# Performance work log

Measured on AMD Instinct MI355X. Metric: run time of the kernel, lower is better.

## Reference

```python
import jax, jax.numpy as jnp
import numpy as np

N = 20000          # nodes
E = 320000         # edges (avg degree 16)
FS = 1000          # feature_size (resnet feature width)
IN = 250 + FS + 250 + 85 * 3  # 1755, actual concat width


def setup_inputs() -> dict:
    key = jax.random.key(0)
    ks = jax.random.split(key, 16)
    # structured node feature matrix x: [layer_id | resnet(1000) | rel_size | rgb(3)]
    layer = jax.random.randint(ks[0], (N, 1), 1, 4).astype(jnp.float32)      # {1,2,3}
    resnet = jax.random.normal(ks[1], (N, FS), jnp.float32)
    rel = jax.random.uniform(ks[2], (N, 1), jnp.float32)                      # [0,1] -> idx 0..10
    colors = jax.random.randint(ks[3], (N, 3), 0, 256).astype(jnp.float32)
    x = jnp.concatenate([layer, resnet, rel, colors], axis=1)  # [N,1005]
    edge_index = jax.random.randint(ks[4], (2, E), 0, N)
    edge_attr = jax.random.uniform(ks[5], (E,), jnp.float32)

    def lin(k, fi, fo):
        return jax.random.normal(k, (fi, fo), jnp.float32) / np.sqrt(fi).astype(np.float32)

    return {
        "x": x,
        "edge_index": edge_index,
        "edge_attr": edge_attr,
        "layer_table": jax.random.normal(ks[6], (3, 250), jnp.float32),
        "rel_table": jax.random.normal(ks[7], (11, 250), jnp.float32),
        "color_table": jax.random.normal(ks[8], (256, 85), jnp.float32),
        "W1": lin(ks[9], IN, 512), "b1": jnp.zeros((512,), jnp.float32),
        "W2": lin(ks[10], 512, 256), "b2": jnp.zeros((256,), jnp.float32),
        "W3": lin(ks[11], 256, 64), "b3": jnp.zeros((64,), jnp.float32),
        "Wp": lin(ks[12], 64, 3), "bp": jnp.zeros((3,), jnp.float32),
    }


def _gcn_conv(h, src, dst, ew, W, b):
    # PyG GCNConv: h' = D^{-1/2} (A + I) D^{-1/2} (h W) + b, with edge weights ew
    h = h @ W
    deg = jax.ops.segment_sum(ew, dst, num_segments=N) + 1.0  # +1 for self-loop weight
    dinv = jnp.where(deg > 0.0, jax.lax.rsqrt(deg), 0.0)
    norm = dinv[src] * ew * dinv[dst]                          # [E]
    agg = jax.ops.segment_sum(h[src] * norm[:, None], dst, num_segments=N)
    agg = agg + h * (dinv * dinv)[:, None]                     # self-loop term
    return agg + b


def reference(x, edge_index, edge_attr, layer_table, rel_table, color_table,
              W1, b1, W2, b2, W3, b3, Wp, bp):
    src, dst = edge_index[0], edge_index[1]
    li = (x[:, 0] - 1.0).astype(jnp.int32)                      # layer id 0..2
    le = layer_table[li]                                        # [N,250]
    resnet = x[:, 1:FS + 1]                                     # [N,1000]
    ri = jnp.round(jnp.abs(x[:, FS + 1]) * 10.0).astype(jnp.int32)
    re = rel_table[ri]                                          # [N,250]
    ci = x[:, -3:].astype(jnp.int32)
    ce = color_table[ci].reshape(x.shape[0], -1)                # [N,255]
    h = jnp.concatenate([le, resnet, re, ce], axis=1)           # [N,1755]

    lrelu = lambda v: jax.nn.leaky_relu(v, 0.01)
    h = lrelu(_gcn_conv(h, src, dst, edge_attr, W1, b1))
    h = lrelu(_gcn_conv(h, src, dst, edge_attr, W2, b2))
    h = lrelu(_gcn_conv(h, src, dst, edge_attr, W3, b3))
    return h @ Wp + bp                                          # [N,3]
```

## Files before the change

### kernel.cpp

```cpp
#include <hip/hip_runtime.h>
#include <hip/hip_bf16.h>

#define NNODES 20000
#define NEDGES 320000
#define XW 1005
#define MP 20096

typedef __attribute__((ext_vector_type(8))) short short8;
typedef __attribute__((ext_vector_type(4))) float f32x4;
typedef __attribute__((ext_vector_type(4))) unsigned short u16x4;

typedef const __attribute__((address_space(1))) short8* g8cp;

__device__ inline void split1(float v, unsigned short& h, unsigned short& l) {
    unsigned u = __float_as_uint(v);
    h = (unsigned short)(u >> 16);
    float hf = __uint_as_float(u & 0xffff0000u);
    l = (unsigned short)(__float_as_uint(v - hf) >> 16);
}

#define PB_EDGE  1250
#define PB_IDX   1329
#define PB_A1    21329
#define PB_BT1   21841
#define PB_BT2   21969
#define PB_BT3   21985
#define PB_TAB   23549

__device__ inline void bt_split_body(int g, const float* __restrict__ W, int ldw,
                                     int koff, int K, int Kp, int Ncols,
                                     unsigned short* __restrict__ Bh,
                                     unsigned short* __restrict__ Bl) {
    int kp4 = Kp >> 2;
    if (g >= Ncols * kp4) return;
    int n = g / kp4, c4 = (g % kp4) << 2;
    u16x4 h, l;
#pragma unroll
    for (int i = 0; i < 4; ++i) {
        int k = c4 + i;
        float v = (k < K) ? W[(size_t)(koff + k) * ldw + n] : 0.0f;
        unsigned short hh, ll;
        split1(v, hh, ll);
        h[i] = (short)hh; l[i] = (short)ll;
    }
    *(u16x4*)&Bh[(size_t)n * Kp + c4] = h;
    *(u16x4*)&Bl[(size_t)n * Kp + c4] = l;
}

__global__ __launch_bounds__(256) void prep_kernel(
    const float* __restrict__ x, const int* __restrict__ ei, const float* __restrict__ ea,
    const float* __restrict__ layer_table, const float* __restrict__ rel_table,
    const float* __restrict__ color_table,
    const float* __restrict__ W1, const float* __restrict__ W2, const float* __restrict__ W3,
    float* __restrict__ deg, int* __restrict__ counts, int* __restrict__ idx8,
    unsigned short* __restrict__ A1h, unsigned short* __restrict__ A1l,
    unsigned short* __restrict__ Bt1h, unsigned short* __restrict__ Bt1l,
    unsigned short* __restrict__ Bt2h, unsigned short* __restrict__ Bt2l,
    unsigned short* __restrict__ Bt3h, unsigned short* __restrict__ Bt3l,
    float* __restrict__ T) {
    const int b = blockIdx.x;
    const int t = threadIdx.x;
    if (b < PB_EDGE) {
        int e = b * 256 + t;
        if (e >= NEDGES) return;
        int dst = ei[NEDGES + e];
        atomicAdd(&deg[dst], ea[e]);
        atomicAdd(&counts[dst], 1);
    } else if (b < PB_IDX) {
        int i = (b - PB_EDGE) * 256 + t;
        if (i >= NNODES) return;
        const float* r = x + (size_t)i * XW;
        idx8[i * 8 + 0] = (int)(r[0] - 1.0f);
        idx8[i * 8 + 1] = (int)rintf(fabsf(r[1001]) * 10.0f);
        idx8[i * 8 + 2] = (int)r[1002];
        idx8[i * 8 + 3] = (int)r[1003];
        idx8[i * 8 + 4] = (int)r[1004];
    } else if (b < PB_A1) {
        int row = b - PB_IDX;
        int c4 = t << 2;
        const float* xp = x + (size_t)row * XW + 1 + c4;
        u16x4 h, l;
#pragma unroll
        for (int i = 0; i < 4; ++i) {
            float v = (c4 + i < 1000) ? xp[i] : 0.0f;
            unsigned short hh, ll;
            split1(v, hh, ll);
            h[i] = (short)hh; l[i] = (short)ll;
        }
        *(u16x4*)&A1h[(size_t)row * 1024 + c4] = h;
        *(u16x4*)&A1l[(size_t)row * 1024 + c4] = l;
    } else if (b < PB_BT1) {
        bt_split_body((b - PB_A1) * 256 + t, W1, 512, 250, 1000, 1024, 512, Bt1h, Bt1l);
    } else if (b < PB_BT2) {
        bt_split_body((b - PB_BT1) * 256 + t, W2, 256, 0, 512, 512, 256, Bt2h, Bt2l);
    } else if (b < PB_BT3) {
        bt_split_body((b - PB_BT2) * 256 + t, W3, 64, 0, 256, 256, 64, Bt3h, Bt3l);
    } else {
        int g = (b - PB_BT3) * 256 + t;
        if (g >= 782 * 512) return;
        int row = g >> 9, col = g & 511;
        float acc = 0.0f;
        if (row < 3) {
            for (int k = 0; k < 250; ++k)
                acc += layer_table[row * 250 + k] * W1[(size_t)k * 512 + col];
        } else if (row < 14) {
            int r = row - 3;
            for (int k = 0; k < 250; ++k)
                acc += rel_table[r * 250 + k] * W1[(size_t)(1250 + k) * 512 + col];
        } else {
            int r = row - 14;
            int j = r >> 8, v = r & 255;
            int base = 1500 + 85 * j;
            for (int k = 0; k < 85; ++k)
                acc += color_table[v * 85 + k] * W1[(size_t)(base + k) * 512 + col];
        }
        T[(size_t)row * 512 + col] = acc;
    }
}


__global__ __launch_bounds__(1024) void scan_p1_kernel(const int* __restrict__ counts,
                                                       int* __restrict__ bsum,
                                                       const float* __restrict__ deg,
                                                       float* __restrict__ dinv, int n) {
    int b = blockIdx.x;
    if (b < 20) {
        __shared__ int ws[16];
        int t = threadIdx.x, lane = t & 63, wid = t >> 6;
        int i = b * 1024 + t;
        int v = (i < n) ? counts[i] : 0;
#pragma unroll
        for (int d = 32; d; d >>= 1) v += __shfl_down(v, d, 64);
        if (lane == 0) ws[wid] = v;
        __syncthreads();
        if (wid == 0) {
            int s = (lane < 16) ? ws[lane] : 0;
#pragma unroll
            for (int d = 8; d; d >>= 1) s += __shfl_down(s, d, 64);
            if (lane == 0) bsum[b] = s;
        }
    } else {
        int i = (b - 20) * 1024 + threadIdx.x;
        if (i < n) { float d = deg[i] + 1.0f; dinv[i] = 1.0f / sqrtf(d); }
    }
}

__global__ void scan_p2_kernel(const int* __restrict__ bsum, int* __restrict__ boffs,
                               int* __restrict__ offs, int n, int nb) {
    int lane = threadIdx.x;
    int v = (lane < nb) ? bsum[lane] : 0;
    int xv = v;
#pragma unroll
    for (int d = 1; d < 64; d <<= 1) {
        int u = __shfl_up(xv, d, 64);
        if (lane >= d) xv += u;
    }
    if (lane < nb) boffs[lane] = xv - v;
    if (lane == nb - 1) offs[n] = xv;
}

__global__ __launch_bounds__(1024) void scan_p3_kernel(const int* __restrict__ counts,
                                                       const int* __restrict__ boffs,
                                                       int* __restrict__ offs, int n) {
    __shared__ int wsum[16], wpre[16];
    int t = threadIdx.x, lane = t & 63, wid = t >> 6;
    int i = blockIdx.x * 1024 + t;
    int v = (i < n) ? counts[i] : 0;
    int xv = v;
#pragma unroll
    for (int d = 1; d < 64; d <<= 1) {
        int u = __shfl_up(xv, d, 64);
        if (lane >= d) xv += u;
    }
    if (lane == 63) wsum[wid] = xv;
    __syncthreads();
    if (wid == 0) {
        int s = (lane < 16) ? wsum[lane] : 0;
#pragma unroll
        for (int d = 1; d < 16; d <<= 1) {
            int u = __shfl_up(s, d, 64);
            if (lane >= d) s += u;
        }
        if (lane < 16) wpre[lane] = s;
    }
    __syncthreads();
    int prefix = boffs[blockIdx.x] + (wid > 0 ? wpre[wid - 1] : 0);
    if (i < n) offs[i] = prefix + xv - v;
}

__global__ void scatter_kernel(const int* __restrict__ ei, const float* __restrict__ ea,
                               const float* __restrict__ dinv, const int* __restrict__ offs,
                               int* __restrict__ cursor, int* __restrict__ csr_src,
                               float* __restrict__ csr_norm, int E) {
    int e = blockIdx.x * 256 + threadIdx.x;
    if (e >= E) return;
    int src = ei[e];
    int dst = ei[E + e];
    int slot = offs[dst] + atomicAdd(&cursor[dst], 1);
    csr_src[slot] = src;
    csr_norm[slot] = dinv[src] * ea[e] * dinv[dst];
}


template <int BN, int NCB, bool EMB>
__global__ __launch_bounds__(256, 3) void gemm_split_kernel(
    const unsigned short* __restrict__ Ah, const unsigned short* __restrict__ Al, int Kp,
    const unsigned short* __restrict__ Bh, const unsigned short* __restrict__ Bl,
    float* __restrict__ C, int ldc, int M,
    const float* __restrict__ T, const int* __restrict__ idx8) {
    constexpr int NT = BN / 32;
    constexpr int BJ = BN / 64;
    __shared__ __align__(16) unsigned short sAh[128 * 32];
    __shared__ __align__(16) unsigned short sAl[128 * 32];
    __shared__ __align__(16) unsigned short sBh[BN * 32];
    __shared__ __align__(16) unsigned short sBl[BN * 32];

    const int t = threadIdx.x;
    const int lane = t & 63;
    const int w = t >> 6;
    const int wr = w >> 1, wc = w & 1;
    const int l15 = lane & 15, quad = lane >> 4;

    const int total = gridDim.x;
    const int per = total >> 3;
    const int bid = blockIdx.x;
    const int tile = (bid < (per << 3)) ? ((bid & 7) * per + (bid >> 3)) : bid;
    const int row0 = (tile / NCB) * 128;
    const int col0 = (tile % NCB) * BN;

    const int si_r = lane >> 2;
    const int si_s = lane & 3;
    const int schunk = si_s ^ ((si_r >> 1) & 3);
    const int sw = (quad ^ ((l15 >> 1) & 3)) * 8;

    const unsigned short* gA[2][2];
    int aoff[2];
#pragma unroll
    for (int j = 0; j < 2; ++j) {
        int ra = w * 32 + j * 16 + si_r;
        size_t e = (size_t)(row0 + ra) * Kp + schunk * 8;
        gA[j][0] = Ah + e; gA[j][1] = Al + e;
        aoff[j] = (w * 32 + j * 16 + si_r) * 32 + si_s * 8;
    }
    const unsigned short* gB[BJ][2];
    int boff[BJ];
#pragma unroll
    for (int j = 0; j < BJ; ++j) {
        int rb = w * (BN / 4) + j * 16 + si_r;
        size_t e = (size_t)(col0 + rb) * Kp + schunk * 8;
        gB[j][0] = Bh + e; gB[j][1] = Bl + e;
        boff[j] = (w * (BN / 4) + j * 16 + si_r) * 32 + si_s * 8;
    }

    f32x4 acc[4][NT];
#pragma unroll
    for (int i = 0; i < 4; ++i)
#pragma unroll
        for (int j = 0; j < NT; ++j)
            acc[i][j] = (f32x4){0.f, 0.f, 0.f, 0.f};

    const int nit = Kp / 32;

    short8 pA[2][2], pB[BJ][2];
#pragma unroll
    for (int j = 0; j < 2; ++j) {
        pA[j][0] = *(g8cp)(const void*)(gA[j][0]);
        pA[j][1] = *(g8cp)(const void*)(gA[j][1]);
    }
#pragma unroll
    for (int j = 0; j < BJ; ++j) {
        pB[j][0] = *(g8cp)(const void*)(gB[j][0]);
        pB[j][1] = *(g8cp)(const void*)(gB[j][1]);
    }

    for (int kt = 0; kt < nit; ++kt) {
#pragma unroll
        for (int j = 0; j < 2; ++j) {
            *(short8*)&sAh[aoff[j]] = pA[j][0];
            *(short8*)&sAl[aoff[j]] = pA[j][1];
        }
#pragma unroll
        for (int j = 0; j < BJ; ++j) {
            *(short8*)&sBh[boff[j]] = pB[j][0];
            *(short8*)&sBl[boff[j]] = pB[j][1];
        }
        if (kt + 1 < nit) {
            const int kb = (kt + 1) * 32;
#pragma unroll
            for (int j = 0; j < 2; ++j) {
                pA[j][0] = *(g8cp)(const void*)(gA[j][0] + kb);
                pA[j][1] = *(g8cp)(const void*)(gA[j][1] + kb);
            }
#pragma unroll
            for (int j = 0; j < BJ; ++j) {
                pB[j][0] = *(g8cp)(const void*)(gB[j][0] + kb);
                pB[j][1] = *(g8cp)(const void*)(gB[j][1] + kb);
            }
        }
        __builtin_amdgcn_s_waitcnt(0xC07F);
        __builtin_amdgcn_s_barrier();
        __builtin_amdgcn_sched_barrier(0);

        short8 fah[4], fal[4], fbh[NT], fbl[NT];
#pragma unroll
        for (int mt = 0; mt < 4; ++mt) {
            int off = (wr * 64 + mt * 16 + l15) * 32 + sw;
            fah[mt] = *(const short8*)&sAh[off];
            fal[mt] = *(const short8*)&sAl[off];
        }
#pragma unroll
        for (int nt = 0; nt < NT; ++nt) {
            int off = (wc * (BN / 2) + nt * 16 + l15) * 32 + sw;
            fbh[nt] = *(const short8*)&sBh[off];
            fbl[nt] = *(const short8*)&sBl[off];
        }
#pragma unroll
        for (int mt = 0; mt < 4; ++mt)
#pragma unroll
            for (int nt = 0; nt < NT; ++nt)
                acc[mt][nt] = __builtin_amdgcn_mfma_f32_16x16x32_bf16(fah[mt], fbh[nt], acc[mt][nt], 0, 0, 0);
#pragma unroll
        for (int mt = 0; mt < 4; ++mt)
#pragma unroll
            for (int nt = 0; nt < NT; ++nt)
                acc[mt][nt] = __builtin_amdgcn_mfma_f32_16x16x32_bf16(fah[mt], fbl[nt], acc[mt][nt], 0, 0, 0);
#pragma unroll
        for (int mt = 0; mt < 4; ++mt)
#pragma unroll
            for (int nt = 0; nt < NT; ++nt)
                acc[mt][nt] = __builtin_amdgcn_mfma_f32_16x16x32_bf16(fal[mt], fbh[nt], acc[mt][nt], 0, 0, 0);
        if (kt + 1 < nit) __builtin_amdgcn_s_barrier();
    }

#pragma unroll
    for (int mt = 0; mt < 4; ++mt)
#pragma unroll
        for (int r = 0; r < 4; ++r) {
            int row = row0 + wr * 64 + mt * 16 + quad * 4 + r;
            if (row >= M) continue;
            if (EMB) {
                const int* ix = idx8 + row * 8;
                const float* t0 = T + (size_t)ix[0] * 512;
                const float* t1 = T + (size_t)(3 + ix[1]) * 512;
                const float* t2 = T + (size_t)(14 + ix[2]) * 512;
                const float* t3 = T + (size_t)(270 + ix[3]) * 512;
                const float* t4 = T + (size_t)(526 + ix[4]) * 512;
#pragma unroll
                for (int nt = 0; nt < NT; ++nt) {
                    int col = col0 + wc * (BN / 2) + nt * 16 + l15;
                    float e = t0[col] + t1[col] + t2[col] + t3[col] + t4[col];
                    C[(size_t)row * ldc + col] = acc[mt][nt][r] + e;
                }
            } else {
#pragma unroll
                for (int nt = 0; nt < NT; ++nt) {
                    int col = col0 + wc * (BN / 2) + nt * 16 + l15;
                    C[(size_t)row * ldc + col] = acc[mt][nt][r];
                }
            }
        }
}


template <int F, int CW, bool SPLIT>
__global__ __launch_bounds__(256) void agg_cols_kernel(
    const float* __restrict__ H, const float* __restrict__ dinv,
    const int* __restrict__ offs, const int* __restrict__ csr_src,
    const float* __restrict__ csr_norm, const float* __restrict__ bias,
    float* __restrict__ outf, unsigned short* __restrict__ Hh,
    unsigned short* __restrict__ Hl, int n_nodes) {
    constexpr int LPN = CW / 4;
    constexpr int NPB = 256 / LPN;
    constexpr int NCH = F / CW;
    constexpr int ECAP = 2048;
    __shared__ int   se[ECAP];
    __shared__ float sn[ECAP];

    const int chunk = blockIdx.x & (NCH - 1);
    const int nb    = blockIdx.x / NCH;
    const int n0 = nb * NPB;
    const int n1 = min(n0 + NPB, n_nodes);
    if (n0 >= n_nodes) return;

    const int estart = offs[n0];
    const int eend   = offs[n1];
    const int ecnt   = eend - estart;
    const bool inlds = (ecnt <= ECAP);
    if (inlds) {
        for (int i = threadIdx.x; i < ecnt; i += 256) {
            se[i] = csr_src[estart + i];
            sn[i] = csr_norm[estart + i];
        }
    }
    __syncthreads();

    const int n = n0 + threadIdx.x / LPN;
    if (n >= n_nodes) return;
    const int lane = threadIdx.x % LPN;
    const int c = chunk * CW + lane * 4;

    float di = dinv[n];
    float s = di * di;
    float4 h = *(const float4*)(H + (size_t)n * F + c);
    float4 acc = make_float4(h.x * s, h.y * s, h.z * s, h.w * s);
    int e0 = offs[n], e1 = offs[n + 1];
    if (inlds) {
        for (int e = e0 - estart; e < e1 - estart; ++e) {
            int src = se[e];
            float w = sn[e];
            float4 v = *(const float4*)(H + (size_t)src * F + c);
            acc.x += v.x * w; acc.y += v.y * w; acc.z += v.z * w; acc.w += v.w * w;
        }
    } else {
        for (int e = e0; e < e1; ++e) {
            int src = csr_src[e];
            float w = csr_norm[e];
            float4 v = *(const float4*)(H + (size_t)src * F + c);
            acc.x += v.x * w; acc.y += v.y * w; acc.z += v.z * w; acc.w += v.w * w;
        }
    }
    float4 b = *(const float4*)(bias + c);
    acc.x += b.x; acc.y += b.y; acc.z += b.z; acc.w += b.w;
    acc.x = acc.x > 0.f ? acc.x : 0.01f * acc.x;
    acc.y = acc.y > 0.f ? acc.y : 0.01f * acc.y;
    acc.z = acc.z > 0.f ? acc.z : 0.01f * acc.z;
    acc.w = acc.w > 0.f ? acc.w : 0.01f * acc.w;
    if (SPLIT) {
        u16x4 hh, ll;
        unsigned short a, bb;
        split1(acc.x, a, bb); hh[0] = (short)a; ll[0] = (short)bb;
        split1(acc.y, a, bb); hh[1] = (short)a; ll[1] = (short)bb;
        split1(acc.z, a, bb); hh[2] = (short)a; ll[2] = (short)bb;
        split1(acc.w, a, bb); hh[3] = (short)a; ll[3] = (short)bb;
        *(u16x4*)(Hh + (size_t)n * F + c) = hh;
        *(u16x4*)(Hl + (size_t)n * F + c) = ll;
    } else {
        *(float4*)(outf + (size_t)n * F + c) = acc;
    }
}


__global__ void proj_kernel(const float* __restrict__ H, const float* __restrict__ Wp,
                            const float* __restrict__ bp, float* __restrict__ out, int n_nodes) {
    int t = blockIdx.x * 192 + threadIdx.x;
    int n = t / 3, j = t % 3;
    if (n >= n_nodes) return;
    float acc = bp[j];
    const float* h = H + (size_t)n * 64;
    for (int c = 0; c < 64; ++c) acc += h[c] * Wp[c * 3 + j];
    out[n * 3 + j] = acc;
}


static inline size_t aln(size_t v) { return (v + 255) & ~(size_t)255; }

extern "C" void kernel_launch(void* const* d_in, const int* in_sizes, int n_in,
                              void* d_out, int out_size, void* d_ws, size_t ws_size,
                              hipStream_t stream) {
    const float* x           = (const float*)d_in[0];
    const int*   edge_index  = (const int*)d_in[1];
    const float* edge_attr   = (const float*)d_in[2];
    const float* layer_table = (const float*)d_in[3];
    const float* rel_table   = (const float*)d_in[4];
    const float* color_table = (const float*)d_in[5];
    const float* W1 = (const float*)d_in[6];
    const float* b1 = (const float*)d_in[7];
    const float* W2 = (const float*)d_in[8];
    const float* b2 = (const float*)d_in[9];
    const float* W3 = (const float*)d_in[10];
    const float* b3 = (const float*)d_in[11];
    const float* Wp = (const float*)d_in[12];
    const float* bp = (const float*)d_in[13];
    float* out = (float*)d_out;

    const int N = NNODES, E = NEDGES;

    char* p = (char*)d_ws;
    float* deg      = (float*)p;
    int*   counts   = (int*)(p + (size_t)N * 4);
    int*   cursor   = (int*)(p + (size_t)N * 8);     p += aln((size_t)N * 12);
    float* dinv     = (float*)p; p += aln((size_t)N * 4);
    float* T        = (float*)p; p += aln((size_t)782 * 512 * 4);
    float* csr_norm = (float*)p; p += aln((size_t)E * 4);
    float* C        = (float*)p; p += aln((size_t)MP * 512 * 4);
    unsigned short* BIG = (unsigned short*)p; p += aln((size_t)MP * 2048 * 2);
    unsigned short* Bt1h = (unsigned short*)p; p += aln((size_t)512 * 1024 * 2);
    unsigned short* Bt1l = (unsigned short*)p; p += aln((size_t)512 * 1024 * 2);
    unsigned short* Bt2h = (unsigned short*)p; p += aln((size_t)256 * 512 * 2);
    unsigned short* Bt2l = (unsigned short*)p; p += aln((size_t)256 * 512 * 2);
    unsigned short* Bt3h = (unsigned short*)p; p += aln((size_t)64 * 256 * 2);
    unsigned short* Bt3l = (unsigned short*)p; p += aln((size_t)64 * 256 * 2);
    int*   csr_src  = (int*)p;   p += aln((size_t)E * 4);
    int*   idx8     = (int*)p;   p += aln((size_t)N * 8 * 4);
    int*   offs     = (int*)p;   p += aln((size_t)(N + 1) * 4);
    int*   bsum     = (int*)p;   p += aln((size_t)32 * 4);
    int*   boffs    = (int*)p;   p += aln((size_t)32 * 4);

    unsigned short* A1h = BIG;
    unsigned short* A1l = BIG + (size_t)MP * 1024;
    unsigned short* H2h = BIG;
    unsigned short* H2l = BIG + (size_t)MP * 512;
    unsigned short* H3h = BIG + (size_t)MP * 1024;
    unsigned short* H3l = BIG + (size_t)MP * 1024 + (size_t)MP * 256;
    float*          H4  = (float*)(BIG + (size_t)MP * 1536);

    hipMemsetAsync(deg, 0, (size_t)N * 12, stream);

    prep_kernel<<<PB_TAB, 256, 0, stream>>>(
        x, edge_index, edge_attr, layer_table, rel_table, color_table,
        W1, W2, W3, deg, counts, idx8,
        A1h, A1l, Bt1h, Bt1l, Bt2h, Bt2l, Bt3h, Bt3l, T);

    scan_p1_kernel<<<40, 1024, 0, stream>>>(counts, bsum, deg, dinv, N);
    scan_p2_kernel<<<1, 64, 0, stream>>>(bsum, boffs, offs, N, 20);
    scan_p3_kernel<<<20, 1024, 0, stream>>>(counts, boffs, offs, N);
    scatter_kernel<<<(E + 255) / 256, 256, 0, stream>>>(edge_index, edge_attr, dinv, offs,
                                                        cursor, csr_src, csr_norm, E);

    const int nrb = MP / 128;

    {
        gemm_split_kernel<128, 4, true><<<nrb * 4, 256, 0, stream>>>(
            A1h, A1l, 1024, Bt1h, Bt1l, C, 512, N, T, idx8);
        int nblocks = (N + 15) / 16;
        agg_cols_kernel<512, 64, true><<<8 * nblocks, 256, 0, stream>>>(
            C, dinv, offs, csr_src, csr_norm, b1, nullptr, H2h, H2l, N);
    }
    {
        gemm_split_kernel<128, 2, false><<<nrb * 2, 256, 0, stream>>>(
            H2h, H2l, 512, Bt2h, Bt2l, C, 256, N, nullptr, nullptr);
        int nblocks = (N + 31) / 32;
        agg_cols_kernel<256, 32, true><<<8 * nblocks, 256, 0, stream>>>(
            C, dinv, offs, csr_src, csr_norm, b2, nullptr, H3h, H3l, N);
    }
    {
        gemm_split_kernel<64, 1, false><<<nrb, 256, 0, stream>>>(
            H3h, H3l, 256, Bt3h, Bt3l, C, 64, N, nullptr, nullptr);
        int nblocks = (N + 63) / 64;
        agg_cols_kernel<64, 16, false><<<4 * nblocks, 256, 0, stream>>>(
            C, dinv, offs, csr_src, csr_norm, b3, H4, nullptr, nullptr, N);
    }
    proj_kernel<<<(N * 3 + 191) / 192, 192, 0, stream>>>(H4, Wp, bp, out, N);
}
```

Baseline: 447.7 us.

## Load GEMM A fragments directly from global, double-buffer B, fuse projection into aggregation

The split-bf16 GEMM stops staging the A tile through shared memory. Each wave now loads its MFMA A fragments straight from global memory, interleaved with the MFMA groups, while B is double-buffered in LDS with a two-step-ahead register prefetch and one barrier per iteration. Separately, the final 64->3 projection is fused into the last aggregation kernel through a lane shuffle reduction, which removes the H4 intermediate and the proj_kernel launch. The direct A loads are uncoalesced per-lane 16-byte reads that rely on cache hits, and the wave is exposed to their global latency inside the MFMA loop.

```diff
diff --git a/kernel.cpp b/kernel.cpp
--- a/kernel.cpp
+++ b/kernel.cpp
@@ -203,17 +203,15 @@
 
 
 template <int BN, int NCB, bool EMB>
-__global__ __launch_bounds__(256, 3) void gemm_split_kernel(
+__global__ __launch_bounds__(256, 3) void gemm_direct_kernel(
     const unsigned short* __restrict__ Ah, const unsigned short* __restrict__ Al, int Kp,
     const unsigned short* __restrict__ Bh, const unsigned short* __restrict__ Bl,
     float* __restrict__ C, int ldc, int M,
     const float* __restrict__ T, const int* __restrict__ idx8) {
     constexpr int NT = BN / 32;
     constexpr int BJ = BN / 64;
-    __shared__ __align__(16) unsigned short sAh[128 * 32];
-    __shared__ __align__(16) unsigned short sAl[128 * 32];
-    __shared__ __align__(16) unsigned short sBh[BN * 32];
-    __shared__ __align__(16) unsigned short sBl[BN * 32];
+    __shared__ __align__(16) unsigned short sBh[2][BN * 32];
+    __shared__ __align__(16) unsigned short sBl[2][BN * 32];
 
     const int t = threadIdx.x;
     const int lane = t & 63;
@@ -233,15 +231,14 @@
     const int schunk = si_s ^ ((si_r >> 1) & 3);
     const int sw = (quad ^ ((l15 >> 1) & 3)) * 8;
 
-    const unsigned short* gA[2][2];
-    int aoff[2];
-#pragma unroll
-    for (int j = 0; j < 2; ++j) {
-        int ra = w * 32 + j * 16 + si_r;
-        size_t e = (size_t)(row0 + ra) * Kp + schunk * 8;
-        gA[j][0] = Ah + e; gA[j][1] = Al + e;
-        aoff[j] = (w * 32 + j * 16 + si_r) * 32 + si_s * 8;
-    }
+    const unsigned short* pAh[4]; const unsigned short* pAl[4];
+#pragma unroll
+    for (int mt = 0; mt < 4; ++mt) {
+        int r = row0 + wr * 64 + mt * 16 + l15;
+        size_t o = (size_t)r * Kp + quad * 8;
+        pAh[mt] = Ah + o; pAl[mt] = Al + o;
+    }
+
     const unsigned short* gB[BJ][2];
     int boff[BJ];
 #pragma unroll
@@ -261,75 +258,99 @@
 
     const int nit = Kp / 32;
 
-    short8 pA[2][2], pB[BJ][2];
-#pragma unroll
-    for (int j = 0; j < 2; ++j) {
-        pA[j][0] = *(g8cp)(const void*)(gA[j][0]);
-        pA[j][1] = *(g8cp)(const void*)(gA[j][1]);
-    }
+    short8 pB[BJ][2];
 #pragma unroll
     for (int j = 0; j < BJ; ++j) {
         pB[j][0] = *(g8cp)(const void*)(gB[j][0]);
         pB[j][1] = *(g8cp)(const void*)(gB[j][1]);
     }
+#pragma unroll
+    for (int j = 0; j < BJ; ++j) {
+        *(short8*)&sBh[0][boff[j]] = pB[j][0];
+        *(short8*)&sBl[0][boff[j]] = pB[j][1];
+    }
+#pragma unroll
+    for (int j = 0; j < BJ; ++j) {
+        pB[j][0] = *(g8cp)(const void*)(gB[j][0] + 32);
+        pB[j][1] = *(g8cp)(const void*)(gB[j][1] + 32);
+    }
+    __builtin_amdgcn_s_waitcnt(0xC07F);
+    __builtin_amdgcn_s_barrier();
+    __builtin_amdgcn_sched_barrier(0);
 
     for (int kt = 0; kt < nit; ++kt) {
-#pragma unroll
-        for (int j = 0; j < 2; ++j) {
-            *(short8*)&sAh[aoff[j]] = pA[j][0];
-            *(short8*)&sAl[aoff[j]] = pA[j][1];
-        }
+        const int cur = kt & 1, nxt = cur ^ 1;
+        const int kbA = kt * 32;
 #pragma unroll
         for (int j = 0; j < BJ; ++j) {
-            *(short8*)&sBh[boff[j]] = pB[j][0];
-            *(short8*)&sBl[boff[j]] = pB[j][1];
-        }
-        if (kt + 1 < nit) {
-            const int kb = (kt + 1) * 32;
-#pragma unroll
-            for (int j = 0; j < 2; ++j) {
-                pA[j][0] = *(g8cp)(const void*)(gA[j][0] + kb);
-                pA[j][1] = *(g8cp)(const void*)(gA[j][1] + kb);
+            *(short8*)&sBh[nxt][boff[j]] = pB[j][0];
+            *(short8*)&sBl[nxt][boff[j]] = pB[j][1];
+        }
+        short8 fa0h = *(g8cp)(const void*)(pAh[0] + kbA);
+        short8 fa0l = *(g8cp)(const void*)(pAl[0] + kbA);
+        short8 fa1h = *(g8cp)(const void*)(pAh[1] + kbA);
+        short8 fa1l = *(g8cp)(const void*)(pAl[1] + kbA);
+        {
+            const int kb2 = (kt + 2 < nit) ? (kt + 2) * 32 : 0;
+#pragma unroll
+            for (int j = 0; j < BJ; ++j) {
+                pB[j][0] = *(g8cp)(const void*)(gB[j][0] + kb2);
+                pB[j][1] = *(g8cp)(const void*)(gB[j][1] + kb2);
             }
-#pragma unroll
-            for (int j = 0; j < BJ; ++j) {
-                pB[j][0] = *(g8cp)(const void*)(gB[j][0] + kb);
-                pB[j][1] = *(g8cp)(const void*)(gB[j][1] + kb);
-            }
-        }
-        __builtin_amdgcn_s_waitcnt(0xC07F);
-        __builtin_amdgcn_s_barrier();
-        __builtin_amdgcn_sched_barrier(0);
-
-        short8 fah[4], fal[4], fbh[NT], fbl[NT];
-#pragma unroll
-        for (int mt = 0; mt < 4; ++mt) {
-            int off = (wr * 64 + mt * 16 + l15) * 32 + sw;
-            fah[mt] = *(const short8*)&sAh[off];
-            fal[mt] = *(const short8*)&sAl[off];
-        }
+        }
+        short8 fbh[NT], fbl[NT];
 #pragma unroll
         for (int nt = 0; nt < NT; ++nt) {
             int off = (wc * (BN / 2) + nt * 16 + l15) * 32 + sw;
-            fbh[nt] = *(const short8*)&sBh[off];
-            fbl[nt] = *(const short8*)&sBl[off];
-        }
-#pragma unroll
-        for (int mt = 0; mt < 4; ++mt)
-#pragma unroll
-            for (int nt = 0; nt < NT; ++nt)
-                acc[mt][nt] = __builtin_amdgcn_mfma_f32_16x16x32_bf16(fah[mt], fbh[nt], acc[mt][nt], 0, 0, 0);
-#pragma unroll
-        for (int mt = 0; mt < 4; ++mt)
-#pragma unroll
-            for (int nt = 0; nt < NT; ++nt)
-                acc[mt][nt] = __builtin_amdgcn_mfma_f32_16x16x32_bf16(fah[mt], fbl[nt], acc[mt][nt], 0, 0, 0);
-#pragma unroll
-        for (int mt = 0; mt < 4; ++mt)
-#pragma unroll
-            for (int nt = 0; nt < NT; ++nt)
-                acc[mt][nt] = __builtin_amdgcn_mfma_f32_16x16x32_bf16(fal[mt], fbh[nt], acc[mt][nt], 0, 0, 0);
-        if (kt + 1 < nit) __builtin_amdgcn_s_barrier();
+            fbh[nt] = *(const short8*)&sBh[cur][off];
+            fbl[nt] = *(const short8*)&sBl[cur][off];
+        }
+#pragma unroll
+        for (int nt = 0; nt < NT; ++nt)
+            acc[0][nt] = __builtin_amdgcn_mfma_f32_16x16x32_bf16(fa0h, fbh[nt], acc[0][nt], 0, 0, 0);
+#pragma unroll
+        for (int nt = 0; nt < NT; ++nt)
+            acc[0][nt] = __builtin_amdgcn_mfma_f32_16x16x32_bf16(fa0h, fbl[nt], acc[0][nt], 0, 0, 0);
+#pragma unroll
+        for (int nt = 0; nt < NT; ++nt)
+            acc[0][nt] = __builtin_amdgcn_mfma_f32_16x16x32_bf16(fa0l, fbh[nt], acc[0][nt], 0, 0, 0);
+        fa0h = *(g8cp)(const void*)(pAh[2] + kbA);
+        fa0l = *(g8cp)(const void*)(pAl[2] + kbA);
+#pragma unroll
+        for (int nt = 0; nt < NT; ++nt)
+            acc[1][nt] = __builtin_amdgcn_mfma_f32_16x16x32_bf16(fa1h, fbh[nt], acc[1][nt], 0, 0, 0);
+#pragma unroll
+        for (int nt = 0; nt < NT; ++nt)
+            acc[1][nt] = __builtin_amdgcn_mfma_f32_16x16x32_bf16(fa1h, fbl[nt], acc[1][nt], 0, 0, 0);
+#pragma unroll
+        for (int nt = 0; nt < NT; ++nt)
+            acc[1][nt] = __builtin_amdgcn_mfma_f32_16x16x32_bf16(fa1l, fbh[nt], acc[1][nt], 0, 0, 0);
+        fa1h = *(g8cp)(const void*)(pAh[3] + kbA);
+        fa1l = *(g8cp)(const void*)(pAl[3] + kbA);
+#pragma unroll
+        for (int nt = 0; nt < NT; ++nt)
+            acc[2][nt] = __builtin_amdgcn_mfma_f32_16x16x32_bf16(fa0h, fbh[nt], acc[2][nt], 0, 0, 0);
+#pragma unroll
+        for (int nt = 0; nt < NT; ++nt)
+            acc[2][nt] = __builtin_amdgcn_mfma_f32_16x16x32_bf16(fa0h, fbl[nt], acc[2][nt], 0, 0, 0);
+#pragma unroll
+        for (int nt = 0; nt < NT; ++nt)
+            acc[2][nt] = __builtin_amdgcn_mfma_f32_16x16x32_bf16(fa0l, fbh[nt], acc[2][nt], 0, 0, 0);
+#pragma unroll
+        for (int nt = 0; nt < NT; ++nt)
+            acc[3][nt] = __builtin_amdgcn_mfma_f32_16x16x32_bf16(fa1h, fbh[nt], acc[3][nt], 0, 0, 0);
+#pragma unroll
+        for (int nt = 0; nt < NT; ++nt)
+            acc[3][nt] = __builtin_amdgcn_mfma_f32_16x16x32_bf16(fa1h, fbl[nt], acc[3][nt], 0, 0, 0);
+#pragma unroll
+        for (int nt = 0; nt < NT; ++nt)
+            acc[3][nt] = __builtin_amdgcn_mfma_f32_16x16x32_bf16(fa1l, fbh[nt], acc[3][nt], 0, 0, 0);
+
+        if (kt + 1 < nit) {
+            __builtin_amdgcn_s_waitcnt(0xC07F);
+            __builtin_amdgcn_s_barrier();
+            __builtin_amdgcn_sched_barrier(0);
+        }
     }
 
 #pragma unroll
@@ -362,13 +383,14 @@
 }
 
 
-template <int F, int CW, bool SPLIT>
+template <int F, int CW, bool SPLIT, bool PROJ>
 __global__ __launch_bounds__(256) void agg_cols_kernel(
     const float* __restrict__ H, const float* __restrict__ dinv,
     const int* __restrict__ offs, const int* __restrict__ csr_src,
     const float* __restrict__ csr_norm, const float* __restrict__ bias,
     float* __restrict__ outf, unsigned short* __restrict__ Hh,
-    unsigned short* __restrict__ Hl, int n_nodes) {
+    unsigned short* __restrict__ Hl,
+    const float* __restrict__ Wp, const float* __restrict__ bp, int n_nodes) {
     constexpr int LPN = CW / 4;
     constexpr int NPB = 256 / LPN;
     constexpr int NCH = F / CW;
@@ -425,7 +447,24 @@
     acc.y = acc.y > 0.f ? acc.y : 0.01f * acc.y;
     acc.z = acc.z > 0.f ? acc.z : 0.01f * acc.z;
     acc.w = acc.w > 0.f ? acc.w : 0.01f * acc.w;
-    if (SPLIT) {
+    if (PROJ) {
+        float p[3];
+#pragma unroll
+        for (int j = 0; j < 3; ++j)
+            p[j] = acc.x * Wp[(c + 0) * 3 + j] + acc.y * Wp[(c + 1) * 3 + j] +
+                   acc.z * Wp[(c + 2) * 3 + j] + acc.w * Wp[(c + 3) * 3 + j];
+#pragma unroll
+        for (int d = 1; d < LPN; d <<= 1) {
+#pragma unroll
+            for (int j = 0; j < 3; ++j)
+                p[j] += __shfl_xor(p[j], d, 64);
+        }
+        if (lane == 0) {
+#pragma unroll
+            for (int j = 0; j < 3; ++j)
+                outf[n * 3 + j] = p[j] + bp[j];
+        }
+    } else if (SPLIT) {
         u16x4 hh, ll;
         unsigned short a, bb;
         split1(acc.x, a, bb); hh[0] = (short)a; ll[0] = (short)bb;
@@ -437,18 +476,6 @@
     } else {
         *(float4*)(outf + (size_t)n * F + c) = acc;
     }
-}
-
-
-__global__ void proj_kernel(const float* __restrict__ H, const float* __restrict__ Wp,
-                            const float* __restrict__ bp, float* __restrict__ out, int n_nodes) {
-    int t = blockIdx.x * 192 + threadIdx.x;
-    int n = t / 3, j = t % 3;
-    if (n >= n_nodes) return;
-    float acc = bp[j];
-    const float* h = H + (size_t)n * 64;
-    for (int c = 0; c < 64; ++c) acc += h[c] * Wp[c * 3 + j];
-    out[n * 3 + j] = acc;
 }
 
 
@@ -502,7 +529,6 @@
     unsigned short* H2l = BIG + (size_t)MP * 512;
     unsigned short* H3h = BIG + (size_t)MP * 1024;
     unsigned short* H3l = BIG + (size_t)MP * 1024 + (size_t)MP * 256;
-    float*          H4  = (float*)(BIG + (size_t)MP * 1536);
 
     hipMemsetAsync(deg, 0, (size_t)N * 12, stream);
 
@@ -520,25 +546,24 @@
     const int nrb = MP / 128;
 
     {
-        gemm_split_kernel<128, 4, true><<<nrb * 4, 256, 0, stream>>>(
+        gemm_direct_kernel<128, 4, true><<<nrb * 4, 256, 0, stream>>>(
             A1h, A1l, 1024, Bt1h, Bt1l, C, 512, N, T, idx8);
         int nblocks = (N + 15) / 16;
-        agg_cols_kernel<512, 64, true><<<8 * nblocks, 256, 0, stream>>>(
-            C, dinv, offs, csr_src, csr_norm, b1, nullptr, H2h, H2l, N);
+        agg_cols_kernel<512, 64, true, false><<<8 * nblocks, 256, 0, stream>>>(
+            C, dinv, offs, csr_src, csr_norm, b1, nullptr, H2h, H2l, nullptr, nullptr, N);
     }
     {
-        gemm_split_kernel<128, 2, false><<<nrb * 2, 256, 0, stream>>>(
+        gemm_direct_kernel<128, 2, false><<<nrb * 2, 256, 0, stream>>>(
             H2h, H2l, 512, Bt2h, Bt2l, C, 256, N, nullptr, nullptr);
         int nblocks = (N + 31) / 32;
-        agg_cols_kernel<256, 32, true><<<8 * nblocks, 256, 0, stream>>>(
-            C, dinv, offs, csr_src, csr_norm, b2, nullptr, H3h, H3l, N);
+        agg_cols_kernel<256, 32, true, false><<<8 * nblocks, 256, 0, stream>>>(
+            C, dinv, offs, csr_src, csr_norm, b2, nullptr, H3h, H3l, nullptr, nullptr, N);
     }
     {
-        gemm_split_kernel<64, 1, false><<<nrb, 256, 0, stream>>>(
+        gemm_direct_kernel<64, 1, false><<<nrb, 256, 0, stream>>>(
             H3h, H3l, 256, Bt3h, Bt3l, C, 64, N, nullptr, nullptr);
-        int nblocks = (N + 63) / 64;
-        agg_cols_kernel<64, 16, false><<<4 * nblocks, 256, 0, stream>>>(
-            C, dinv, offs, csr_src, csr_norm, b3, H4, nullptr, nullptr, N);
-    }
-    proj_kernel<<<(N * 3 + 191) / 192, 192, 0, stream>>>(H4, Wp, bp, out, N);
-}
+        int nblocks = (N + 15) / 16;
+        agg_cols_kernel<64, 64, false, true><<<nblocks, 256, 0, stream>>>(
+            C, dinv, offs, csr_src, csr_norm, b3, out, nullptr, nullptr, Wp, bp, N);
+    }
+}
```

Result: slower. 524.1 us (+17.1%).
